# Kernel tuning notes

Measured on AMD Instinct MI355X. Metric: run time of the kernel, lower is better.

The kernel has to match this reference:

```python
import jax, jax.numpy as jnp
import numpy as np

DIM = 1024
HIDDEN = 1024
NUM_EXPERTS = 8
TOP_K = 2


def setup_inputs() -> dict:
    key = jax.random.key(0)
    ks = jax.random.split(key, 8)
    std = 0.02
    x = jax.random.normal(ks[0], (2, 1024, DIM), dtype=jnp.float32)
    gate_w = jax.random.normal(ks[1], (NUM_EXPERTS, DIM), dtype=jnp.float32) * std
    w1 = jax.random.normal(ks[2], (NUM_EXPERTS, DIM, HIDDEN), dtype=jnp.float32) * std
    w2 = jax.random.normal(ks[3], (NUM_EXPERTS, HIDDEN, DIM), dtype=jnp.float32) * std
    w3 = jax.random.normal(ks[4], (NUM_EXPERTS, DIM, HIDDEN), dtype=jnp.float32) * std
    w1s = jax.random.normal(ks[5], (1, DIM, HIDDEN), dtype=jnp.float32) * std
    w2s = jax.random.normal(ks[6], (1, HIDDEN, DIM), dtype=jnp.float32) * std
    w3s = jax.random.normal(ks[7], (1, DIM, HIDDEN), dtype=jnp.float32) * std
    return {"x": x, "gate_w": gate_w, "w1": w1, "w2": w2, "w3": w3,
            "w1s": w1s, "w2s": w2s, "w3s": w3s}


def reference(x, gate_w, w1, w2, w3, w1s, w2s, w3s):
    bs, slen, dim = x.shape
    xt = x.reshape(bs * slen, dim)                       # [N, d]

    # ---- token-choice top-k router (softmax in fp32) ----
    logits = xt @ gate_w.T                               # [N, E]
    scores = jax.nn.softmax(logits.astype(jnp.float32), axis=1).astype(x.dtype)
    top_scores, sel = jax.lax.top_k(scores, TOP_K)       # [N, K]
    sel_flat = sel.reshape(-1)                           # [N*K]
    order = jnp.argsort(sel_flat, stable=True)           # sort tokens by expert
    top_scores_sorted = top_scores.reshape(-1)[order]    # [T]
    token_idx = order // TOP_K                           # [T] source token per routed row
    eid = sel_flat[order]                                # [T] expert id per routed row

    # ---- dispatch: gather + pre-scale by router score ----
    routed_in = xt[token_idx] * top_scores_sorted[:, None]   # [T, d]

    # ---- grouped SwiGLU experts (fixed loop over experts, masked) ----
    out_routed = jnp.zeros_like(routed_in)
    for e in range(NUM_EXPERTS):
        m = (eid == e)[:, None]
        xe = jnp.where(m, routed_in, 0.0)
        h = jax.nn.silu(xe @ w1[e]) * (xe @ w3[e])
        out_routed = out_routed + jnp.where(m, h @ w2[e], 0.0)

    # ---- shared expert over all tokens ----
    hs = jax.nn.silu(xt @ w1s[0]) * (xt @ w3s[0])
    out = hs @ w2s[0]                                    # [N, d]

    # ---- combine: scatter-add routed outputs ----
    out = out.at[token_idx].add(out_routed)
    return out.reshape(bs, slen, dim)
```

## Files before the change

kernel.cpp:

```cpp
#include <hip/hip_runtime.h>
#include <hip/hip_bf16.h>


#define DIM 1024
#define NTOK 2048
#define NEXP 8
#define NENT 4096
#define ROWS_CAP 8192
#define MAX_TILES 64
#define MM (DIM * DIM)

typedef float f32x4 __attribute__((ext_vector_type(4)));
typedef __bf16 bf16x8 __attribute__((ext_vector_type(8)));

__device__ __forceinline__ unsigned short f2bf(float f) {
  unsigned int u = __builtin_bit_cast(unsigned int, f);
  unsigned int r = u + 0x7FFFu + ((u >> 16) & 1u);
  return (unsigned short)(r >> 16);
}
__device__ __forceinline__ float bf2f(unsigned short h) {
  unsigned int u = ((unsigned int)h) << 16;
  return __builtin_bit_cast(float, u);
}
__device__ __forceinline__ void gload_lds16(const unsigned short* g, unsigned short* l) {
  __builtin_amdgcn_global_load_lds((__attribute__((address_space(1))) const void*)g,
                                   (__attribute__((address_space(3))) void*)l, 16, 0, 0);
}

__device__ __forceinline__ void brick_transpose(const float* __restrict__ src,
                                                unsigned short* __restrict__ dst,
                                                int n_blk, int k_blk,
                                                unsigned short* lds) {
  int c0 = n_blk * 128, r0 = k_blk * 128;
  int tid = threadIdx.x;
  int q = tid & 31;
  int kq0 = tid >> 5;

  const float* sp0 = src + (size_t)(r0 + kq0 * 4) * DIM + c0 + q * 4;
  const float* sp1 = sp0 + (size_t)64 * DIM;
  float4 v0 = *(const float4*)(sp0 + 0 * DIM);
  float4 v1 = *(const float4*)(sp0 + 1 * DIM);
  float4 v2 = *(const float4*)(sp0 + 2 * DIM);
  float4 v3 = *(const float4*)(sp0 + 3 * DIM);
  float4 v4 = *(const float4*)(sp1 + 0 * DIM);
  float4 v5 = *(const float4*)(sp1 + 1 * DIM);
  float4 v6 = *(const float4*)(sp1 + 2 * DIM);
  float4 v7 = *(const float4*)(sp1 + 3 * DIM);
  {
    float a0[4] = {v0.x, v0.y, v0.z, v0.w};
    float a1[4] = {v1.x, v1.y, v1.z, v1.w};
    float a2[4] = {v2.x, v2.y, v2.z, v2.w};
    float a3[4] = {v3.x, v3.y, v3.z, v3.w};
    float b0[4] = {v4.x, v4.y, v4.z, v4.w};
    float b1[4] = {v5.x, v5.y, v5.z, v5.w};
    float b2[4] = {v6.x, v6.y, v6.z, v6.w};
    float b3[4] = {v7.x, v7.y, v7.z, v7.w};
#pragma unroll
    for (int j = 0; j < 4; j++) {
      int row = q * 4 + j;
      {
        int kq = kq0;
        int ch = kq >> 1, half = kq & 1;
        unsigned int off = (unsigned int)row * 128 + ((ch ^ (row & 15)) * 8 + half * 4);
        uint2 p;
        p.x = f2bf(a0[j]) | ((unsigned int)f2bf(a1[j]) << 16);
        p.y = f2bf(a2[j]) | ((unsigned int)f2bf(a3[j]) << 16);
        *(uint2*)(lds + off) = p;
      }
      {
        int kq = kq0 + 16;
        int ch = kq >> 1, half = kq & 1;
        unsigned int off = (unsigned int)row * 128 + ((ch ^ (row & 15)) * 8 + half * 4);
        uint2 p;
        p.x = f2bf(b0[j]) | ((unsigned int)f2bf(b1[j]) << 16);
        p.y = f2bf(b2[j]) | ((unsigned int)f2bf(b3[j]) << 16);
        *(uint2*)(lds + off) = p;
      }
    }
  }
  __syncthreads();

  size_t bbase = ((size_t)n_blk * 32 + (size_t)k_blk * 4) * 4096;
#pragma unroll
  for (int i = 0; i < 4; i++) {
    int g = tid + i * 512;
    int kcr = g >> 9;
    int c = g & 511;
    int row = c >> 2, p = c & 3;
    int koff = (p - (row >> 1)) & 3;
    int ch = kcr * 4 + koff;
    uint4 val = *(const uint4*)(lds + (unsigned int)row * 128 + (ch ^ (row & 15)) * 8);
    *(uint4*)(dst + bbase + (size_t)g * 8) = val;
  }
}

__global__ __launch_bounds__(512) void t13_router(
    const float* __restrict__ x, const float* __restrict__ gw,
    const float* __restrict__ w1, const float* __restrict__ w3,
    const float* __restrict__ w1s, const float* __restrict__ w3s,
    unsigned short* __restrict__ w1t, unsigned short* __restrict__ w3t,
    unsigned short* __restrict__ w1st, unsigned short* __restrict__ w3st,
    unsigned short* __restrict__ xbf,
    int* __restrict__ e0, int* __restrict__ e1,
    float* __restrict__ s0, float* __restrict__ s1) {
  __shared__ __align__(16) unsigned short lds[128 * 128];
  int b = blockIdx.x;
  if (b < 256) {
    int lane = threadIdx.x & 63;
    int t = b * 8 + (threadIdx.x >> 6);
    const float4* xr4 = (const float4*)(x + (size_t)t * DIM);
    float4 xv[4];
#pragma unroll
    for (int i = 0; i < 4; i++) xv[i] = xr4[i * 64 + lane];

    ushort4* xb4 = (ushort4*)(xbf + (size_t)t * DIM);
#pragma unroll
    for (int i = 0; i < 4; i++) {
      ushort4 o;
      o.x = f2bf(xv[i].x); o.y = f2bf(xv[i].y); o.z = f2bf(xv[i].z); o.w = f2bf(xv[i].w);
      xb4[i * 64 + lane] = o;
    }
    if (t == 0) {
      ushort4 zz; zz.x = zz.y = zz.z = zz.w = 0;
      ushort4* pb4 = (ushort4*)(xbf + (size_t)NTOK * DIM);
#pragma unroll
      for (int i = 0; i < 4; i++) pb4[i * 64 + lane] = zz;
    }

    float acc[NEXP];
#pragma unroll
    for (int e = 0; e < NEXP; e++) {
      const float4* g4 = (const float4*)(gw + (size_t)e * DIM);
      float a = 0.f;
#pragma unroll
      for (int i = 0; i < 4; i++) {
        float4 g = g4[i * 64 + lane];
        a += xv[i].x * g.x + xv[i].y * g.y + xv[i].z * g.z + xv[i].w * g.w;
      }
      acc[e] = a;
    }
#pragma unroll
    for (int e = 0; e < NEXP; e++) {
      float v = acc[e];
      for (int o = 32; o > 0; o >>= 1) v += __shfl_xor(v, o);
      acc[e] = v;
    }
    if (lane == 0) {
      float m = acc[0];
#pragma unroll
      for (int e = 1; e < NEXP; e++) m = fmaxf(m, acc[e]);
      float ex[NEXP]; float Z = 0.f;
#pragma unroll
      for (int e = 0; e < NEXP; e++) { ex[e] = __expf(acc[e] - m); Z += ex[e]; }
      float inv = 1.f / Z;
      float sc[NEXP];
#pragma unroll
      for (int e = 0; e < NEXP; e++) sc[e] = ex[e] * inv;
      int b0 = 0; float v0 = sc[0];
#pragma unroll
      for (int e = 1; e < NEXP; e++) if (sc[e] > v0) { v0 = sc[e]; b0 = e; }
      int b1 = -1; float v1 = -1.f;
#pragma unroll
      for (int e = 0; e < NEXP; e++) if (e != b0 && sc[e] > v1) { v1 = sc[e]; b1 = e; }
      e0[t] = b0; e1[t] = b1; s0[t] = v0; s1[t] = v1;
    }
  } else {
    int bb = b - 256;
    int slice = bb >> 6, s6 = bb & 63;
    int n_blk = s6 & 7, k_blk = s6 >> 3;
    const float* src; unsigned short* dst;
    if (slice < 5)       { src = w1 + (size_t)(slice + 3) * MM; dst = w1t + (size_t)(slice + 3) * MM; }
    else if (slice < 13) { src = w3 + (size_t)(slice - 5) * MM; dst = w3t + (size_t)(slice - 5) * MM; }
    else if (slice == 13){ src = w1s; dst = w1st; }
    else                 { src = w3s; dst = w3st; }
    brick_transpose(src, dst, n_blk, k_blk, lds);
  }
}

__global__ __launch_bounds__(512) void build_t(
    const int* __restrict__ e0, const int* __restrict__ e1,
    const float* __restrict__ s0, const float* __restrict__ s1,
    const float* __restrict__ w1, unsigned short* __restrict__ w1t,
    int* __restrict__ gtok, float* __restrict__ gsc, int* __restrict__ row_of,
    int* __restrict__ tile_e, int* __restrict__ tile_r0, int* __restrict__ ntiles,
    int* __restrict__ base8out) {
  __shared__ __align__(16) unsigned short lds[128 * 128];
  __shared__ unsigned int wsum[4][4];
  __shared__ int offl[256][NEXP];
  __shared__ int lrl[256][NEXP];

  int b = blockIdx.x;
  if (b > 0) {
    int bb = b - 1;
    int slice = bb >> 6, s6 = bb & 63;
    brick_transpose(w1 + (size_t)slice * MM, w1t + (size_t)slice * MM,
                    s6 & 7, s6 >> 3, lds);
    return;
  }

  int t = threadIdx.x, lane = t & 63, wave = t >> 6;
  bool act = t < 256;

  for (int i = t; i < ROWS_CAP; i += 512) { gtok[i] = NTOK; gsc[i] = 0.f; }

  unsigned int pc[4] = {0, 0, 0, 0};
  if (act) {
#pragma unroll
    for (int i = 0; i < 16; i++) {
      int ent = t * 16 + i;
      int tok = ent >> 1;
      int e = (ent & 1) ? e1[tok] : e0[tok];
      unsigned int add = 1u << ((e & 1) * 16);
      int c = e >> 1;
      if (c == 0) pc[0] += add; else if (c == 1) pc[1] += add;
      else if (c == 2) pc[2] += add; else pc[3] += add;
    }
  }
  unsigned int incl[4] = {pc[0], pc[1], pc[2], pc[3]};
#pragma unroll
  for (int o = 1; o < 64; o <<= 1) {
    unsigned int u0 = __shfl_up(incl[0], o), u1 = __shfl_up(incl[1], o);
    unsigned int u2 = __shfl_up(incl[2], o), u3 = __shfl_up(incl[3], o);
    if (lane >= o) { incl[0] += u0; incl[1] += u1; incl[2] += u2; incl[3] += u3; }
  }
  if (act && lane == 63) { wsum[wave][0] = incl[0]; wsum[wave][1] = incl[1];
                           wsum[wave][2] = incl[2]; wsum[wave][3] = incl[3]; }
  __syncthreads();
  unsigned int T[4], pre[4] = {0, 0, 0, 0};
#pragma unroll
  for (int c = 0; c < 4; c++)
    T[c] = wsum[0][c] + wsum[1][c] + wsum[2][c] + wsum[3][c];
#pragma unroll
  for (int w = 0; w < 3; w++)
    if (wave > w) { pre[0] += wsum[w][0]; pre[1] += wsum[w][1];
                    pre[2] += wsum[w][2]; pre[3] += wsum[w][3]; }
  int base[NEXP + 1];
  {
    int bsum = 0;
#pragma unroll
    for (int e = 0; e < NEXP; e++) {
      int tot = (int)((T[e >> 1] >> ((e & 1) * 16)) & 0xFFFFu);
      base[e] = bsum; bsum += (tot + 127) & ~127;
    }
    base[NEXP] = bsum;
  }
  if (act) {
#pragma unroll
    for (int e = 0; e < NEXP; e++) {
      unsigned int ex = (incl[e >> 1] + pre[e >> 1] - pc[e >> 1]);
      offl[t][e] = (int)((ex >> ((e & 1) * 16)) & 0xFFFFu);
      lrl[t][e] = 0;
    }
  }
  if (t == 0) {
    int nt = 0;
#pragma unroll
    for (int e = 0; e < NEXP; e++) {
      int tot = (int)((T[e >> 1] >> ((e & 1) * 16)) & 0xFFFFu);
      int ntl = (tot + 127) >> 7;
      for (int i = 0; i < ntl; i++) { tile_e[nt] = e; tile_r0[nt] = base[e] + i * 128; nt++; }
    }
    for (int i = 0; i < NTOK / 128; i++) { tile_e[nt] = NEXP; tile_r0[nt] = base[NEXP] + i * 128; nt++; }
    *ntiles = nt;
    *base8out = base[NEXP];
  }
  __syncthreads();

  if (act) {
#pragma unroll
    for (int i = 0; i < 16; i++) {
      int ent = t * 16 + i;
      int tok = ent >> 1;
      int k = ent & 1;
      int e = k ? e1[tok] : e0[tok];
      float s = k ? s1[tok] : s0[tok];
      int pos = base[e] + offl[t][e] + lrl[t][e];
      lrl[t][e]++;
      gtok[pos] = tok; gsc[pos] = s; row_of[ent] = pos;
    }
  }
  for (int i = t; i < NTOK; i += 512) { gtok[base[NEXP] + i] = i; gsc[base[NEXP] + i] = 1.0f; }
}

__global__ __launch_bounds__(512, 4) void gemm13_t2(
    const unsigned short* __restrict__ xbf,
    const unsigned short* __restrict__ W1, const unsigned short* __restrict__ W1s,
    const unsigned short* __restrict__ W3, const unsigned short* __restrict__ W3s,
    const float* __restrict__ w2, const float* __restrict__ w2s,
    unsigned short* __restrict__ w2t, unsigned short* __restrict__ w2st,
    unsigned short* __restrict__ H,
    const int* __restrict__ gtok, const float* __restrict__ gsc,
    const int* __restrict__ tile_e, const int* __restrict__ tile_r0,
    const int* __restrict__ ntiles) {
  __shared__ __align__(16) char smem[49664];
  int b = blockIdx.x;
  if (b >= 512) {
    int bb = b - 512;
    int slice = bb >> 6, s6 = bb & 63;
    int n_blk = s6 & 7, k_blk = s6 >> 3;
    const float* src; unsigned short* dst;
    if (slice < 8) { src = w2 + (size_t)slice * MM; dst = w2t + (size_t)slice * MM; }
    else           { src = w2s; dst = w2st; }
    brick_transpose(src, dst, n_blk, k_blk, (unsigned short*)smem);
    return;
  }
  int ti = b >> 3;
  if (ti >= *ntiles) return;
  int e = tile_e[ti];
  int row0 = tile_r0[ti];
  int col0 = (b & 7) * 128;
  const unsigned short* B1 = (e < NEXP) ? (W1 + (size_t)e * MM) : W1s;
  const unsigned short* B3 = (e < NEXP) ? (W3 + (size_t)e * MM) : W3s;

  unsigned short* As  = (unsigned short*)smem;
  unsigned short* Bs1 = (unsigned short*)(smem + 16384);
  unsigned short* Bs3 = (unsigned short*)(smem + 32768);
  float* ss = (float*)(smem + 49152);

  int tid = threadIdx.x;
  int wave = tid >> 6, lane = tid & 63;
  int wrow = (wave >> 2) * 64, wcol = (wave & 3) * 32;

  if (tid < 128) ss[tid] = gsc[row0 + tid];

  f32x4 acc1[4][2], acc3[4][2];
#pragma unroll
  for (int m = 0; m < 4; m++)
#pragma unroll
    for (int n = 0; n < 2; n++) { acc1[m][n] = f32x4{0.f,0.f,0.f,0.f}; acc3[m][n] = f32x4{0.f,0.f,0.f,0.f}; }

  int arow = tid >> 2;
  int akoff = (((tid & 3) - (arow >> 1)) & 3) * 8;
  const unsigned short* ga  = xbf + (size_t)gtok[row0 + arow] * DIM + akoff;
  const unsigned short* gb1 = B1 + ((size_t)(col0 >> 7) * 32) * 4096 + (size_t)tid * 8;
  const unsigned short* gb3 = B3 + ((size_t)(col0 >> 7) * 32) * 4096 + (size_t)tid * 8;
  unsigned short* lA  = As  + wave * 512;
  unsigned short* lB1 = Bs1 + wave * 512;
  unsigned short* lB3 = Bs3 + wave * 512;

  int kc = lane >> 4, rl = lane & 15;

  for (int it = 0; it < 16; it++) {
    int k0 = it * 64;
    size_t boff = (size_t)(it * 2) * 4096;
    gload_lds16(ga + k0,      lA);
    gload_lds16(ga + k0 + 32, lA + 4096);
    gload_lds16(gb1 + boff,        lB1);
    gload_lds16(gb1 + boff + 4096, lB1 + 4096);
    gload_lds16(gb3 + boff,        lB3);
    gload_lds16(gb3 + boff + 4096, lB3 + 4096);
    __syncthreads();

#pragma unroll
    for (int h = 0; h < 2; h++) {
      const bf16x8* Ap  = (const bf16x8*)As  + h * 512;
      const bf16x8* B1p = (const bf16x8*)Bs1 + h * 512;
      const bf16x8* B3p = (const bf16x8*)Bs3 + h * 512;
      bf16x8 af[4], b1f[2], b3f[2];
#pragma unroll
      for (int m = 0; m < 4; m++) {
        int row = wrow + m * 16 + rl;
        af[m] = Ap[row * 4 + ((kc + (row >> 1)) & 3)];
      }
#pragma unroll
      for (int n = 0; n < 2; n++) {
        int row = wcol + n * 16 + rl;
        int p = row * 4 + ((kc + (row >> 1)) & 3);
        b1f[n] = B1p[p];
        b3f[n] = B3p[p];
      }
      __builtin_amdgcn_s_setprio(1);
#pragma unroll
      for (int m = 0; m < 4; m++)
#pragma unroll
        for (int n = 0; n < 2; n++) {
          acc1[m][n] = __builtin_amdgcn_mfma_f32_16x16x32_bf16(af[m], b1f[n], acc1[m][n], 0, 0, 0);
          acc3[m][n] = __builtin_amdgcn_mfma_f32_16x16x32_bf16(af[m], b3f[n], acc3[m][n], 0, 0, 0);
        }
      __builtin_amdgcn_s_setprio(0);
    }
    __syncthreads();
  }

  int rj = lane >> 4, cl = lane & 15;
#pragma unroll
  for (int m = 0; m < 4; m++)
#pragma unroll
    for (int n = 0; n < 2; n++)
#pragma unroll
      for (int j = 0; j < 4; j++) {
        int lr = wrow + m * 16 + rj * 4 + j;
        float s = ss[lr];
        float a = s * acc1[m][n][j];
        float g = s * acc3[m][n][j];
        float si = a / (1.f + __expf(-a));
        H[(size_t)(row0 + lr) * DIM + (col0 + wcol + n * 16 + cl)] = f2bf(si * g);
      }
}

__global__ __launch_bounds__(512, 4) void gemm2(
    const unsigned short* __restrict__ A, const unsigned short* __restrict__ W,
    const unsigned short* __restrict__ Wsh, unsigned short* __restrict__ C,
    const int* __restrict__ tile_e, const int* __restrict__ tile_r0,
    const int* __restrict__ ntiles) {
  if ((int)blockIdx.y >= *ntiles) return;
  int e = tile_e[blockIdx.y];
  int row0 = tile_r0[blockIdx.y];
  int col0 = blockIdx.x * 128;
  const unsigned short* B = (e < NEXP) ? (W + (size_t)e * MM) : Wsh;

  __shared__ __align__(16) unsigned short As[2 * 4096];
  __shared__ __align__(16) unsigned short Bs[2 * 4096];

  int tid = threadIdx.x;
  int wave = tid >> 6, lane = tid & 63;
  int wrow = (wave & 3) * 32, wcol = (wave >> 2) * 64;

  f32x4 acc[2][4];
#pragma unroll
  for (int m = 0; m < 2; m++)
#pragma unroll
    for (int n = 0; n < 4; n++) acc[m][n] = f32x4{0.f, 0.f, 0.f, 0.f};

  int arow = tid >> 2;
  int akoff = (((tid & 3) - (arow >> 1)) & 3) * 8;
  const unsigned short* ga = A + (size_t)(row0 + arow) * DIM + akoff;
  const unsigned short* gb = B + ((size_t)(col0 >> 7) * 32) * 4096 + (size_t)tid * 8;
  unsigned short* lA = As + wave * 512;
  unsigned short* lB = Bs + wave * 512;

  int kc = lane >> 4, rl = lane & 15;

  for (int it = 0; it < 16; it++) {
    int k0 = it * 64;
    size_t boff = (size_t)(it * 2) * 4096;
    gload_lds16(ga + k0,      lA);
    gload_lds16(ga + k0 + 32, lA + 4096);
    gload_lds16(gb + boff,        lB);
    gload_lds16(gb + boff + 4096, lB + 4096);
    __syncthreads();

#pragma unroll
    for (int h = 0; h < 2; h++) {
      const bf16x8* Ap = (const bf16x8*)As + h * 512;
      const bf16x8* Bp = (const bf16x8*)Bs + h * 512;
      bf16x8 af[2], bfr[4];
#pragma unroll
      for (int m = 0; m < 2; m++) {
        int row = wrow + m * 16 + rl;
        af[m] = Ap[row * 4 + ((kc + (row >> 1)) & 3)];
      }
#pragma unroll
      for (int n = 0; n < 4; n++) {
        int row = wcol + n * 16 + rl;
        bfr[n] = Bp[row * 4 + ((kc + (row >> 1)) & 3)];
      }
#pragma unroll
      for (int m = 0; m < 2; m++)
#pragma unroll
        for (int n = 0; n < 4; n++)
          acc[m][n] = __builtin_amdgcn_mfma_f32_16x16x32_bf16(af[m], bfr[n], acc[m][n], 0, 0, 0);
    }
    __syncthreads();
  }

  int rj = lane >> 4, cl = lane & 15;
#pragma unroll
  for (int m = 0; m < 2; m++)
#pragma unroll
    for (int n = 0; n < 4; n++)
#pragma unroll
      for (int j = 0; j < 4; j++) {
        int r = row0 + wrow + m * 16 + rj * 4 + j;
        int c = col0 + wcol + n * 16 + cl;
        C[(size_t)r * DIM + c] = f2bf(acc[m][n][j]);
      }
}

__global__ __launch_bounds__(256) void combine(const unsigned short* __restrict__ routb,
                                               const int* __restrict__ row_of,
                                               const int* __restrict__ base8,
                                               float* __restrict__ out) {
  int t = blockIdx.x;
  int c = threadIdx.x * 4;
  int r0 = row_of[2 * t], r1 = row_of[2 * t + 1];
  int rs = *base8 + t;
  ushort4 v0 = *(const ushort4*)(routb + (size_t)r0 * DIM + c);
  ushort4 v1 = *(const ushort4*)(routb + (size_t)r1 * DIM + c);
  ushort4 v2 = *(const ushort4*)(routb + (size_t)rs * DIM + c);
  float4 o;
  o.x = bf2f(v0.x) + bf2f(v1.x) + bf2f(v2.x);
  o.y = bf2f(v0.y) + bf2f(v1.y) + bf2f(v2.y);
  o.z = bf2f(v0.z) + bf2f(v1.z) + bf2f(v2.z);
  o.w = bf2f(v0.w) + bf2f(v1.w) + bf2f(v2.w);
  *(float4*)(out + (size_t)t * DIM + c) = o;
}

extern "C" void kernel_launch(void* const* d_in, const int* in_sizes, int n_in,
                              void* d_out, int out_size, void* d_ws, size_t ws_size,
                              hipStream_t stream) {
  const float* x   = (const float*)d_in[0];
  const float* gw  = (const float*)d_in[1];
  const float* w1  = (const float*)d_in[2];
  const float* w2  = (const float*)d_in[3];
  const float* w3  = (const float*)d_in[4];
  const float* w1s = (const float*)d_in[5];
  const float* w2s = (const float*)d_in[6];
  const float* w3s = (const float*)d_in[7];
  float* out = (float*)d_out;
  char* ws = (char*)d_ws;

  const size_t MB = 1ull << 20;
  unsigned short* w1t  = (unsigned short*)(ws + 0 * MB);
  unsigned short* w3t  = (unsigned short*)(ws + 16 * MB);
  unsigned short* w2t  = (unsigned short*)(ws + 32 * MB);
  unsigned short* w1st = (unsigned short*)(ws + 48 * MB);
  unsigned short* w3st = (unsigned short*)(ws + 50 * MB);
  unsigned short* w2st = (unsigned short*)(ws + 52 * MB);
  unsigned short* xbf  = (unsigned short*)(ws + 54 * MB);
  unsigned short* hbuf = (unsigned short*)(ws + 60 * MB);
  unsigned short* routb= (unsigned short*)(ws + 76 * MB);
  char* meta = ws + 108 * MB;
  int*   e0p    = (int*)meta;
  int*   e1p    = e0p + NTOK;
  float* s0p    = (float*)(e1p + NTOK);
  float* s1p    = s0p + NTOK;
  int*   gtok   = (int*)(s1p + NTOK);
  float* gsc    = (float*)(gtok + ROWS_CAP);
  int*   row_of = (int*)(gsc + ROWS_CAP);
  int*   tile_e = row_of + NENT;
  int*   tile_r0= tile_e + MAX_TILES;
  int*   ntiles = tile_r0 + MAX_TILES;
  int*   base8  = ntiles + 1;

  t13_router<<<256 + 15 * 64, 512, 0, stream>>>(
      x, gw, w1, w3, w1s, w3s, w1t, w3t, w1st, w3st, xbf, e0p, e1p, s0p, s1p);
  build_t<<<1 + 3 * 64, 512, 0, stream>>>(e0p, e1p, s0p, s1p, w1, w1t,
                                          gtok, gsc, row_of, tile_e, tile_r0, ntiles, base8);
  gemm13_t2<<<512 + 9 * 64, 512, 0, stream>>>(
      xbf, w1t, w1st, w3t, w3st, w2, w2s, w2t, w2st, hbuf,
      gtok, gsc, tile_e, tile_r0, ntiles);
  dim3 gg(8, MAX_TILES);
  gemm2<<<gg, 512, 0, stream>>>(hbuf, w2t, w2st, routb, tile_e, tile_r0, ntiles);
  combine<<<NTOK, 256, 0, stream>>>(routb, row_of, base8, out);
}
```

Baseline: 94.31 us.

## Transpose four weight bricks per block with register double-buffered loads

The fp32-to-bf16 weight transpose now handles four 128x128 bricks per block instead of one. The next brick's global loads are issued into a second register set before the current brick is packed into LDS and written out, so load latency overlaps the LDS and store phases. The transpose grid shrinks by four, and launch_bounds(512,2) is added to the router and build kernels. This trades per-block parallelism and register pressure for fewer blocks and better latency hiding. Transposing weights on every call was already present before this change.

```diff
diff --git a/kernel.cpp b/kernel.cpp
--- a/kernel.cpp
+++ b/kernel.cpp
@@ -94,7 +94,82 @@
   }
 }
 
-__global__ __launch_bounds__(512) void t13_router(
+#define BT4_LOAD(V, NB)                                                       \
+  { const float* sp0_ = src + (size_t)(r0 + kq0 * 4) * DIM + (NB) * 128 + q * 4; \
+    const float* sp1_ = sp0_ + (size_t)64 * DIM;                              \
+    V[0] = *(const float4*)(sp0_ + 0 * DIM);                                  \
+    V[1] = *(const float4*)(sp0_ + 1 * DIM);                                  \
+    V[2] = *(const float4*)(sp0_ + 2 * DIM);                                  \
+    V[3] = *(const float4*)(sp0_ + 3 * DIM);                                  \
+    V[4] = *(const float4*)(sp1_ + 0 * DIM);                                  \
+    V[5] = *(const float4*)(sp1_ + 1 * DIM);                                  \
+    V[6] = *(const float4*)(sp1_ + 2 * DIM);                                  \
+    V[7] = *(const float4*)(sp1_ + 3 * DIM); }
+
+#define BT4_PACK(V)                                                           \
+  { float a0_[4] = {V[0].x, V[0].y, V[0].z, V[0].w};                          \
+    float a1_[4] = {V[1].x, V[1].y, V[1].z, V[1].w};                          \
+    float a2_[4] = {V[2].x, V[2].y, V[2].z, V[2].w};                          \
+    float a3_[4] = {V[3].x, V[3].y, V[3].z, V[3].w};                          \
+    float b0_[4] = {V[4].x, V[4].y, V[4].z, V[4].w};                          \
+    float b1_[4] = {V[5].x, V[5].y, V[5].z, V[5].w};                          \
+    float b2_[4] = {V[6].x, V[6].y, V[6].z, V[6].w};                          \
+    float b3_[4] = {V[7].x, V[7].y, V[7].z, V[7].w};                          \
+    _Pragma("unroll")                                                         \
+    for (int j = 0; j < 4; j++) {                                             \
+      int row = q * 4 + j;                                                    \
+      { int ch = kq0 >> 1, half = kq0 & 1;                                    \
+        unsigned int off = (unsigned int)row * 128 + ((ch ^ (row & 15)) * 8 + half * 4); \
+        uint2 p_;                                                             \
+        p_.x = f2bf(a0_[j]) | ((unsigned int)f2bf(a1_[j]) << 16);             \
+        p_.y = f2bf(a2_[j]) | ((unsigned int)f2bf(a3_[j]) << 16);             \
+        *(uint2*)(lds + off) = p_; }                                          \
+      { int kq = kq0 + 16; int ch = kq >> 1, half = kq & 1;                   \
+        unsigned int off = (unsigned int)row * 128 + ((ch ^ (row & 15)) * 8 + half * 4); \
+        uint2 p_;                                                             \
+        p_.x = f2bf(b0_[j]) | ((unsigned int)f2bf(b1_[j]) << 16);             \
+        p_.y = f2bf(b2_[j]) | ((unsigned int)f2bf(b3_[j]) << 16);             \
+        *(uint2*)(lds + off) = p_; } } }
+
+#define BT4_FENCE                                            \
+  { asm volatile("s_waitcnt lgkmcnt(0)" ::: "memory");       \
+    __builtin_amdgcn_s_barrier(); }
+
+#define BT4_PHASE2(NB)                                                        \
+  { size_t bbase_ = ((size_t)(NB) * 32 + (size_t)k_blk * 4) * 4096;           \
+    _Pragma("unroll")                                                         \
+    for (int i = 0; i < 4; i++) {                                             \
+      int g = tid + i * 512;                                                  \
+      int kcr = g >> 9;                                                       \
+      int c = g & 511;                                                        \
+      int row = c >> 2, p = c & 3;                                            \
+      int koff = (p - (row >> 1)) & 3;                                        \
+      int ch = kcr * 4 + koff;                                                \
+      uint4 val = *(const uint4*)(lds + (unsigned int)row * 128 + (ch ^ (row & 15)) * 8); \
+      *(uint4*)(dst + bbase_ + (size_t)g * 8) = val;                          \
+    } }
+
+__device__ __forceinline__ void brick_transpose4(const float* __restrict__ src,
+                                                 unsigned short* __restrict__ dst,
+                                                 int k_blk, int nb0,
+                                                 unsigned short* lds) {
+  int tid = threadIdx.x;
+  int q = tid & 31;
+  int kq0 = tid >> 5;
+  int r0 = k_blk * 128;
+  float4 va[8], vb[8];
+
+  BT4_LOAD(va, nb0 + 0);
+  BT4_LOAD(vb, nb0 + 1);
+  BT4_PACK(va);  BT4_FENCE;  BT4_PHASE2(nb0 + 0);  BT4_FENCE;
+  BT4_LOAD(va, nb0 + 2);
+  BT4_PACK(vb);  BT4_FENCE;  BT4_PHASE2(nb0 + 1);  BT4_FENCE;
+  BT4_LOAD(vb, nb0 + 3);
+  BT4_PACK(va);  BT4_FENCE;  BT4_PHASE2(nb0 + 2);  BT4_FENCE;
+  BT4_PACK(vb);  BT4_FENCE;  BT4_PHASE2(nb0 + 3);
+}
+
+__global__ __launch_bounds__(512, 2) void t13_router(
     const float* __restrict__ x, const float* __restrict__ gw,
     const float* __restrict__ w1, const float* __restrict__ w3,
     const float* __restrict__ w1s, const float* __restrict__ w3s,
@@ -166,18 +241,18 @@
     }
   } else {
     int bb = b - 256;
-    int slice = bb >> 6, s6 = bb & 63;
-    int n_blk = s6 & 7, k_blk = s6 >> 3;
+    int slice = bb >> 4, s16 = bb & 15;
+    int k_blk = s16 >> 1, nb0 = (s16 & 1) * 4;
     const float* src; unsigned short* dst;
     if (slice < 5)       { src = w1 + (size_t)(slice + 3) * MM; dst = w1t + (size_t)(slice + 3) * MM; }
     else if (slice < 13) { src = w3 + (size_t)(slice - 5) * MM; dst = w3t + (size_t)(slice - 5) * MM; }
     else if (slice == 13){ src = w1s; dst = w1st; }
     else                 { src = w3s; dst = w3st; }
-    brick_transpose(src, dst, n_blk, k_blk, lds);
-  }
-}
-
-__global__ __launch_bounds__(512) void build_t(
+    brick_transpose4(src, dst, k_blk, nb0, lds);
+  }
+}
+
+__global__ __launch_bounds__(512, 2) void build_t(
     const int* __restrict__ e0, const int* __restrict__ e1,
     const float* __restrict__ s0, const float* __restrict__ s1,
     const float* __restrict__ w1, unsigned short* __restrict__ w1t,
@@ -192,9 +267,9 @@
   int b = blockIdx.x;
   if (b > 0) {
     int bb = b - 1;
-    int slice = bb >> 6, s6 = bb & 63;
-    brick_transpose(w1 + (size_t)slice * MM, w1t + (size_t)slice * MM,
-                    s6 & 7, s6 >> 3, lds);
+    int slice = bb >> 4, s16 = bb & 15;
+    brick_transpose4(w1 + (size_t)slice * MM, w1t + (size_t)slice * MM,
+                     s16 >> 1, (s16 & 1) * 4, lds);
     return;
   }
 
@@ -533,9 +608,9 @@
   int*   ntiles = tile_r0 + MAX_TILES;
   int*   base8  = ntiles + 1;
 
-  t13_router<<<256 + 15 * 64, 512, 0, stream>>>(
+  t13_router<<<256 + 15 * 16, 512, 0, stream>>>(
       x, gw, w1, w3, w1s, w3s, w1t, w3t, w1st, w3st, xbf, e0p, e1p, s0p, s1p);
-  build_t<<<1 + 3 * 64, 512, 0, stream>>>(e0p, e1p, s0p, s1p, w1, w1t,
+  build_t<<<1 + 3 * 16, 512, 0, stream>>>(e0p, e1p, s0p, s1p, w1, w1t,
                                           gtok, gsc, row_of, tile_e, tile_r0, ntiles, base8);
   gemm13_t2<<<512 + 9 * 64, 512, 0, stream>>>(
       xbf, w1t, w1st, w3t, w3st, w2, w2s, w2t, w2st, hbuf,
```

Result: no change. 93.51 us, median of 2 (-0.9%).
